# Kernel tuning notes

Measured on AMD Instinct MI355X. Metric: run time of the kernel, lower is better.

Reference implementation:

```python
import jax, jax.numpy as jnp
import numpy as np

B = 8192
T = 100       # repeat_vector
I = 30        # input_size
H = 100       # hidden_size


def setup_inputs() -> dict:
    key = jax.random.key(0)
    ks = jax.random.split(key, 7)
    k = 1.0 / np.sqrt(H)  # torch LSTM/Linear init scale
    u = lambda kk, shape: jax.random.uniform(kk, shape, jnp.float32, -k, k)
    return {
        "x": jax.random.normal(ks[0], (B, I), jnp.float32),
        "W_ih": u(ks[1], (4 * H, I)),   # gate order: i, f, g, o
        "W_hh": u(ks[2], (4 * H, H)),
        "b_ih": u(ks[3], (4 * H,)),
        "b_hh": u(ks[4], (4 * H,)),
        "W_d": u(ks[5], (1, H)),
        "b_d": u(ks[6], (1,)),
    }


def _lstm_dense(x, W_ih, W_hh, b_ih, b_hh, W_d, b_d):
    # Input is the same vector at every timestep (repeat), so project once.
    xp = x @ W_ih.T + b_ih + b_hh  # [B, 4H]
    h0 = jnp.zeros((x.shape[0], H), x.dtype)
    c0 = jnp.zeros((x.shape[0], H), x.dtype)

    def step(carry, _):
        h, c = carry
        gates = xp + h @ W_hh.T                      # [B, 4H]
        i, f, g, o = jnp.split(gates, 4, axis=-1)
        i = jax.nn.sigmoid(i)
        f = jax.nn.sigmoid(f)
        g = jnp.tanh(g)
        o = jax.nn.sigmoid(o)
        c = f * c + i * g
        h = o * jnp.tanh(c)
        return (h, c), h

    _, hs = jax.lax.scan(step, (h0, c0), None, length=T)  # [T, B, H]
    hs = jnp.transpose(hs, (1, 0, 2))                     # [B, T, H]
    return hs @ W_d.T + b_d                               # [B, T, 1]


def reference(x, W_ih, W_hh, b_ih, b_hh, W_d, b_d):
    return _lstm_dense(x, W_ih, W_hh, b_ih, b_hh, W_d, b_d)
```

## Files before the change

kernel.cpp:

```cpp
#include <hip/hip_runtime.h>


#define LOG2E 1.44269504088896340736f

typedef _Float16 f16x8 __attribute__((ext_vector_type(8)));
typedef float    f32x4 __attribute__((ext_vector_type(4)));

__device__ __forceinline__ float rcp_(float x) { return __builtin_amdgcn_rcpf(x); }
__device__ __forceinline__ float exp2_(float x) { return __builtin_amdgcn_exp2f(x); }

__device__ __forceinline__ unsigned pk_f16(float a, float b) {
    return __builtin_bit_cast(unsigned, __builtin_amdgcn_cvt_pkrtz(a, b));
}

#define KS 136

__global__ __launch_bounds__(256, 2) void lstm_kernel(
    const float* __restrict__ x, const float* __restrict__ Wih,
    const float* __restrict__ Whh, const float* __restrict__ bih,
    const float* __restrict__ bhh, const float* __restrict__ Wd,
    const float* __restrict__ bd, float* __restrict__ out)
{
    __shared__ __align__(16) _Float16 Wstg[128 * KS];
    __shared__ __align__(16) _Float16 hlds[2][16 * KS];
    __shared__ float outb[16 * 100];

    const int tid = threadIdx.x;
    const int w   = tid >> 6;
    const int l   = tid & 63;
    const int g   = l >> 4;
    const int c   = l & 15;
    const int b0  = blockIdx.x * 16;
    const bool wpo = (w == 3) && (c == 2);

    for (int i = tid; i < 128 * KS / 2; i += 256) ((unsigned*)Wstg)[i] = 0u;
    for (int i = tid; i < 2 * 16 * KS / 2; i += 256) ((unsigned*)&hlds[0][0])[i] = 0u;
    __syncthreads();

    f16x8 wfrag[2][4][4];
    for (int s = 0; s < 4; ++s) {
        const float sc = (s == 2) ? (-2.0f * LOG2E) : (-LOG2E);
        for (int idx = tid; idx < 10000; idx += 256) {
            int uu = idx / 100, k = idx - uu * 100;
            int col = 32 * (uu >> 5) + 16 * (uu & 1) + ((uu & 31) >> 1);
            Wstg[col * KS + k] = (_Float16)(Whh[(s * 100 + uu) * 100 + k] * sc);
        }
        if (s == 0)
            for (int k = tid; k < 100; k += 256)
                Wstg[98 * KS + k] = (_Float16)Wd[k];
        __syncthreads();
        #pragma unroll
        for (int nt = 0; nt < 2; ++nt)
            #pragma unroll
            for (int ks = 0; ks < 4; ++ks)
                wfrag[nt][s][ks] = *(const f16x8*)
                    &Wstg[(w * 32 + nt * 16 + c) * KS + ks * 32 + g * 8];
        __syncthreads();
    }

    const int row0 = b0 + 4 * g;
    f32x4 xq[2][4];
    float creg[2][4];
    #pragma unroll
    for (int nt = 0; nt < 2; ++nt) {
        #pragma unroll
        for (int s = 0; s < 4; ++s) xq[nt][s] = (f32x4){0.f, 0.f, 0.f, 0.f};
        #pragma unroll
        for (int r = 0; r < 4; ++r) creg[nt][r] = 0.0f;
    }
    for (int k = 0; k < 30; ++k) {
        float xv[4];
        #pragma unroll
        for (int r = 0; r < 4; ++r) xv[r] = x[(row0 + r) * 30 + k];
        #pragma unroll
        for (int nt = 0; nt < 2; ++nt) {
            int u = w * 32 + 2 * c + nt;
            if (u < 100) {
                #pragma unroll
                for (int s = 0; s < 4; ++s) {
                    float wv = Wih[(s * 100 + u) * 30 + k];
                    #pragma unroll
                    for (int r = 0; r < 4; ++r) xq[nt][s][r] += xv[r] * wv;
                }
            }
        }
    }
    #pragma unroll
    for (int nt = 0; nt < 2; ++nt) {
        int u = w * 32 + 2 * c + nt;
        if (u < 100) {
            #pragma unroll
            for (int s = 0; s < 4; ++s) {
                float sc = (s == 2) ? (-2.0f * LOG2E) : (-LOG2E);
                float b  = bih[s * 100 + u] + bhh[s * 100 + u];
                #pragma unroll
                for (int r = 0; r < 4; ++r)
                    xq[nt][s][r] = (xq[nt][s][r] + b) * sc;
            }
        }
    }
    const float bdv = bd[0];
    __syncthreads();

    const int afb = c * KS + g * 8;
    const int hwc = w * 32 + 2 * c;

#define STEP(P, TCUR)                                                          \
    {                                                                          \
        const _Float16* hr = &hlds[(P)][0];                                    \
        _Float16*       hw = &hlds[(P) ^ 1][0];                                \
        f16x8 af[4];                                                           \
        _Pragma("unroll")                                                      \
        for (int ks = 0; ks < 4; ++ks)                                         \
            af[ks] = *(const f16x8*)&hr[afb + ks * 32];                        \
               \
        f32x4 acc[2][4];                                                       \
        _Pragma("unroll")                                                      \
        for (int nt = 0; nt < 2; ++nt)                                         \
            _Pragma("unroll")                                                  \
            for (int s = 0; s < 4; ++s)                                        \
                acc[nt][s] = __builtin_amdgcn_mfma_f32_16x16x32_f16(           \
                        af[0], wfrag[nt][s][0], xq[nt][s], 0, 0, 0);           \
        _Pragma("unroll")                                                      \
        for (int ks = 1; ks < 4; ++ks)                                         \
            _Pragma("unroll")                                                  \
            for (int nt = 0; nt < 2; ++nt)                                     \
                _Pragma("unroll")                                              \
                for (int s = 0; s < 4; ++s)                                    \
                    acc[nt][s] = __builtin_amdgcn_mfma_f32_16x16x32_f16(       \
                            af[ks], wfrag[nt][s][ks], acc[nt][s], 0, 0, 0);    \
              \
        if ((TCUR) > 0 && wpo) {                                               \
            _Pragma("unroll")                                                  \
            for (int r = 0; r < 4; ++r)                                        \
                outb[(4 * g + r) * 100 + (TCUR) - 1] = acc[0][0][r] + bdv;     \
        }                                                                      \
                   \
        _Pragma("unroll")                                                      \
        for (int r = 0; r < 4; ++r) {                                          \
            float hv[2];                                                       \
            _Pragma("unroll")                                                  \
            for (int nt = 0; nt < 2; ++nt) {                                   \
                float A  = exp2_(acc[nt][0][r]);                               \
                float F  = exp2_(acc[nt][1][r]);                               \
                float G  = exp2_(acc[nt][2][r]);                               \
                float O  = exp2_(acc[nt][3][r]);                               \
                float a1 = 1.0f + A, f1 = 1.0f + F;                            \
                float g1 = 1.0f + G, gm = 1.0f - G;                            \
                float ag  = a1 * g1;                                           \
                float num = fmaf(creg[nt][r], ag, gm * f1);                    \
                float cg  = num * rcp_(ag * f1);                               \
                creg[nt][r] = cg;                                              \
                float C2 = exp2_(cg * (-2.0f * LOG2E));                        \
                hv[nt] = (1.0f - C2) * rcp_((1.0f + O) * (1.0f + C2));         \
            }                                                                  \
            *(unsigned*)&hw[(4 * g + r) * KS + hwc] = pk_f16(hv[0], hv[1]);    \
        }                                                                      \
        __syncthreads();                                                       \
    }

    for (int t2 = 0; t2 < 50; ++t2) {
        STEP(0, 2 * t2);
        STEP(1, 2 * t2 + 1);
    }
#undef STEP

    {
        f16x8 af[4];
        #pragma unroll
        for (int ks = 0; ks < 4; ++ks)
            af[ks] = *(const f16x8*)&hlds[0][afb + ks * 32];
        f32x4 a = {0.f, 0.f, 0.f, 0.f};
        #pragma unroll
        for (int ks = 0; ks < 4; ++ks)
            a = __builtin_amdgcn_mfma_f32_16x16x32_f16(
                    af[ks], wfrag[0][0][ks], a, 0, 0, 0);
        if (wpo) {
            #pragma unroll
            for (int r = 0; r < 4; ++r)
                outb[(4 * g + r) * 100 + 99] = a[r] + bdv;
        }
    }
    __syncthreads();
    for (int i = tid; i < 1600; i += 256)
        out[b0 * 100 + i] = outb[i];
}

extern "C" void kernel_launch(void* const* d_in, const int* in_sizes, int n_in,
                              void* d_out, int out_size, void* d_ws, size_t ws_size,
                              hipStream_t stream) {
    (void)in_sizes; (void)n_in; (void)out_size; (void)d_ws; (void)ws_size;
    const float* x   = (const float*)d_in[0];
    const float* Wih = (const float*)d_in[1];
    const float* Whh = (const float*)d_in[2];
    const float* bih = (const float*)d_in[3];
    const float* bhh = (const float*)d_in[4];
    const float* Wd  = (const float*)d_in[5];
    const float* bd  = (const float*)d_in[6];
    lstm_kernel<<<dim3(512), dim3(256), 0, stream>>>(
        x, Wih, Whh, bih, bhh, Wd, bd, (float*)d_out);
}
```

Measured before the change: 172.8 us.

## Process two 16-row batch tiles per block sharing register-resident weight fragments

Each block now handles 32 batch rows as two independent 16-row MFMA tiles that reuse the same W_hh fragments held in registers. The grid is halved to 256 blocks and launch bounds drop to one block per SIMD group. This gives two independent MFMA chains and activation streams per step to hide latency, and halves the number of barriers per row and the per-block weight staging. The cost is higher register pressure and fewer resident waves, and 256 blocks may leave some of the GPU's compute units idle.

```diff
diff --git a/kernel.cpp b/kernel.cpp
--- a/kernel.cpp
+++ b/kernel.cpp
@@ -15,26 +15,26 @@
 
 #define KS 136
 
-__global__ __launch_bounds__(256, 2) void lstm_kernel(
+__global__ __launch_bounds__(256, 1) void lstm_kernel(
     const float* __restrict__ x, const float* __restrict__ Wih,
     const float* __restrict__ Whh, const float* __restrict__ bih,
     const float* __restrict__ bhh, const float* __restrict__ Wd,
     const float* __restrict__ bd, float* __restrict__ out)
 {
     __shared__ __align__(16) _Float16 Wstg[128 * KS];
-    __shared__ __align__(16) _Float16 hlds[2][16 * KS];
-    __shared__ float outb[16 * 100];
+    __shared__ __align__(16) _Float16 hlds[2][32 * KS];
+    __shared__ float outb[32 * 100];
 
     const int tid = threadIdx.x;
     const int w   = tid >> 6;
     const int l   = tid & 63;
     const int g   = l >> 4;
     const int c   = l & 15;
-    const int b0  = blockIdx.x * 16;
+    const int b0  = blockIdx.x * 32;
     const bool wpo = (w == 3) && (c == 2);
 
     for (int i = tid; i < 128 * KS / 2; i += 256) ((unsigned*)Wstg)[i] = 0u;
-    for (int i = tid; i < 2 * 16 * KS / 2; i += 256) ((unsigned*)&hlds[0][0])[i] = 0u;
+    for (int i = tid; i < 2 * 32 * KS / 2; i += 256) ((unsigned*)&hlds[0][0])[i] = 0u;
     __syncthreads();
 
     f16x8 wfrag[2][4][4];
@@ -58,20 +58,25 @@
         __syncthreads();
     }
 
-    const int row0 = b0 + 4 * g;
-    f32x4 xq[2][4];
-    float creg[2][4];
+    f32x4 xqX[2][4], xqY[2][4];
+    float cregX[2][4], cregY[2][4];
     #pragma unroll
     for (int nt = 0; nt < 2; ++nt) {
         #pragma unroll
-        for (int s = 0; s < 4; ++s) xq[nt][s] = (f32x4){0.f, 0.f, 0.f, 0.f};
-        #pragma unroll
-        for (int r = 0; r < 4; ++r) creg[nt][r] = 0.0f;
+        for (int s = 0; s < 4; ++s) {
+            xqX[nt][s] = (f32x4){0.f, 0.f, 0.f, 0.f};
+            xqY[nt][s] = (f32x4){0.f, 0.f, 0.f, 0.f};
+        }
+        #pragma unroll
+        for (int r = 0; r < 4; ++r) { cregX[nt][r] = 0.0f; cregY[nt][r] = 0.0f; }
     }
     for (int k = 0; k < 30; ++k) {
-        float xv[4];
-        #pragma unroll
-        for (int r = 0; r < 4; ++r) xv[r] = x[(row0 + r) * 30 + k];
+        float xvX[4], xvY[4];
+        #pragma unroll
+        for (int r = 0; r < 4; ++r) {
+            xvX[r] = x[(b0 + 4 * g + r) * 30 + k];
+            xvY[r] = x[(b0 + 16 + 4 * g + r) * 30 + k];
+        }
         #pragma unroll
         for (int nt = 0; nt < 2; ++nt) {
             int u = w * 32 + 2 * c + nt;
@@ -80,7 +85,10 @@
                 for (int s = 0; s < 4; ++s) {
                     float wv = Wih[(s * 100 + u) * 30 + k];
                     #pragma unroll
-                    for (int r = 0; r < 4; ++r) xq[nt][s][r] += xv[r] * wv;
+                    for (int r = 0; r < 4; ++r) {
+                        xqX[nt][s][r] += xvX[r] * wv;
+                        xqY[nt][s][r] += xvY[r] * wv;
+                    }
                 }
             }
         }
@@ -94,68 +102,82 @@
                 float sc = (s == 2) ? (-2.0f * LOG2E) : (-LOG2E);
                 float b  = bih[s * 100 + u] + bhh[s * 100 + u];
                 #pragma unroll
-                for (int r = 0; r < 4; ++r)
-                    xq[nt][s][r] = (xq[nt][s][r] + b) * sc;
+                for (int r = 0; r < 4; ++r) {
+                    xqX[nt][s][r] = (xqX[nt][s][r] + b) * sc;
+                    xqY[nt][s][r] = (xqY[nt][s][r] + b) * sc;
+                }
             }
         }
     }
     const float bdv = bd[0];
     __syncthreads();
 
-    const int afb = c * KS + g * 8;
-    const int hwc = w * 32 + 2 * c;
+    const int afbX = c * KS + g * 8;
+    const int afbY = (16 + c) * KS + g * 8;
+    const int hwc  = w * 32 + 2 * c;
+
+#define TILE_ACTS(ACC, CREG, HW, ROWOFF)                                       \
+    _Pragma("unroll")                                                          \
+    for (int r = 0; r < 4; ++r) {                                              \
+        float hv[2];                                                           \
+        _Pragma("unroll")                                                      \
+        for (int nt = 0; nt < 2; ++nt) {                                       \
+            float A  = exp2_(ACC[nt][0][r]);                                   \
+            float F  = exp2_(ACC[nt][1][r]);                                   \
+            float G  = exp2_(ACC[nt][2][r]);                                   \
+            float O  = exp2_(ACC[nt][3][r]);                                   \
+            float a1 = 1.0f + A, f1 = 1.0f + F;                                \
+            float g1 = 1.0f + G, gm = 1.0f - G;                                \
+            float ag  = a1 * g1;                                               \
+            float num = fmaf(CREG[nt][r], ag, gm * f1);                        \
+            float cg  = num * rcp_(ag * f1);                                   \
+            CREG[nt][r] = cg;                                                  \
+            float C2 = exp2_(cg * (-2.0f * LOG2E));                            \
+            hv[nt] = (1.0f - C2) * rcp_((1.0f + O) * (1.0f + C2));             \
+        }                                                                      \
+        *(unsigned*)&HW[((ROWOFF) + 4 * g + r) * KS + hwc] = pk_f16(hv[0], hv[1]); \
+    }
 
 #define STEP(P, TCUR)                                                          \
     {                                                                          \
         const _Float16* hr = &hlds[(P)][0];                                    \
         _Float16*       hw = &hlds[(P) ^ 1][0];                                \
-        f16x8 af[4];                                                           \
-        _Pragma("unroll")                                                      \
-        for (int ks = 0; ks < 4; ++ks)                                         \
-            af[ks] = *(const f16x8*)&hr[afb + ks * 32];                        \
-               \
-        f32x4 acc[2][4];                                                       \
+        f16x8 afX[4], afY[4];                                                  \
+        _Pragma("unroll")                                                      \
+        for (int ks = 0; ks < 4; ++ks) {                                       \
+            afX[ks] = *(const f16x8*)&hr[afbX + ks * 32];                      \
+            afY[ks] = *(const f16x8*)&hr[afbY + ks * 32];                      \
+        }                                                                      \
+        f32x4 accX[2][4], accY[2][4];                                          \
         _Pragma("unroll")                                                      \
         for (int nt = 0; nt < 2; ++nt)                                         \
             _Pragma("unroll")                                                  \
-            for (int s = 0; s < 4; ++s)                                        \
-                acc[nt][s] = __builtin_amdgcn_mfma_f32_16x16x32_f16(           \
-                        af[0], wfrag[nt][s][0], xq[nt][s], 0, 0, 0);           \
+            for (int s = 0; s < 4; ++s) {                                      \
+                accX[nt][s] = __builtin_amdgcn_mfma_f32_16x16x32_f16(          \
+                        afX[0], wfrag[nt][s][0], xqX[nt][s], 0, 0, 0);         \
+                accY[nt][s] = __builtin_amdgcn_mfma_f32_16x16x32_f16(          \
+                        afY[0], wfrag[nt][s][0], xqY[nt][s], 0, 0, 0);         \
+            }                                                                  \
         _Pragma("unroll")                                                      \
         for (int ks = 1; ks < 4; ++ks)                                         \
             _Pragma("unroll")                                                  \
             for (int nt = 0; nt < 2; ++nt)                                     \
                 _Pragma("unroll")                                              \
-                for (int s = 0; s < 4; ++s)                                    \
-                    acc[nt][s] = __builtin_amdgcn_mfma_f32_16x16x32_f16(       \
-                            af[ks], wfrag[nt][s][ks], acc[nt][s], 0, 0, 0);    \
-              \
+                for (int s = 0; s < 4; ++s) {                                  \
+                    accX[nt][s] = __builtin_amdgcn_mfma_f32_16x16x32_f16(      \
+                            afX[ks], wfrag[nt][s][ks], accX[nt][s], 0, 0, 0);  \
+                    accY[nt][s] = __builtin_amdgcn_mfma_f32_16x16x32_f16(      \
+                            afY[ks], wfrag[nt][s][ks], accY[nt][s], 0, 0, 0);  \
+                }                                                              \
         if ((TCUR) > 0 && wpo) {                                               \
             _Pragma("unroll")                                                  \
-            for (int r = 0; r < 4; ++r)                                        \
-                outb[(4 * g + r) * 100 + (TCUR) - 1] = acc[0][0][r] + bdv;     \
+            for (int r = 0; r < 4; ++r) {                                      \
+                outb[(4 * g + r) * 100 + (TCUR) - 1] = accX[0][0][r] + bdv;    \
+                outb[(16 + 4 * g + r) * 100 + (TCUR) - 1] = accY[0][0][r] + bdv; \
+            }                                                                  \
         }                                                                      \
-                   \
-        _Pragma("unroll")                                                      \
-        for (int r = 0; r < 4; ++r) {                                          \
-            float hv[2];                                                       \
-            _Pragma("unroll")                                                  \
-            for (int nt = 0; nt < 2; ++nt) {                                   \
-                float A  = exp2_(acc[nt][0][r]);                               \
-                float F  = exp2_(acc[nt][1][r]);                               \
-                float G  = exp2_(acc[nt][2][r]);                               \
-                float O  = exp2_(acc[nt][3][r]);                               \
-                float a1 = 1.0f + A, f1 = 1.0f + F;                            \
-                float g1 = 1.0f + G, gm = 1.0f - G;                            \
-                float ag  = a1 * g1;                                           \
-                float num = fmaf(creg[nt][r], ag, gm * f1);                    \
-                float cg  = num * rcp_(ag * f1);                               \
-                creg[nt][r] = cg;                                              \
-                float C2 = exp2_(cg * (-2.0f * LOG2E));                        \
-                hv[nt] = (1.0f - C2) * rcp_((1.0f + O) * (1.0f + C2));         \
-            }                                                                  \
-            *(unsigned*)&hw[(4 * g + r) * KS + hwc] = pk_f16(hv[0], hv[1]);    \
-        }                                                                      \
+        TILE_ACTS(accX, cregX, hw, 0)                                          \
+        TILE_ACTS(accY, cregY, hw, 16)                                         \
         __syncthreads();                                                       \
     }
 
@@ -164,25 +186,31 @@
         STEP(1, 2 * t2 + 1);
     }
 #undef STEP
+#undef TILE_ACTS
 
     {
-        f16x8 af[4];
-        #pragma unroll
-        for (int ks = 0; ks < 4; ++ks)
-            af[ks] = *(const f16x8*)&hlds[0][afb + ks * 32];
-        f32x4 a = {0.f, 0.f, 0.f, 0.f};
-        #pragma unroll
-        for (int ks = 0; ks < 4; ++ks)
-            a = __builtin_amdgcn_mfma_f32_16x16x32_f16(
-                    af[ks], wfrag[0][0][ks], a, 0, 0, 0);
+        f16x8 afX[4], afY[4];
+        #pragma unroll
+        for (int ks = 0; ks < 4; ++ks) {
+            afX[ks] = *(const f16x8*)&hlds[0][afbX + ks * 32];
+            afY[ks] = *(const f16x8*)&hlds[0][afbY + ks * 32];
+        }
+        f32x4 aX = {0.f, 0.f, 0.f, 0.f}, aY = {0.f, 0.f, 0.f, 0.f};
+        #pragma unroll
+        for (int ks = 0; ks < 4; ++ks) {
+            aX = __builtin_amdgcn_mfma_f32_16x16x32_f16(afX[ks], wfrag[0][0][ks], aX, 0, 0, 0);
+            aY = __builtin_amdgcn_mfma_f32_16x16x32_f16(afY[ks], wfrag[0][0][ks], aY, 0, 0, 0);
+        }
         if (wpo) {
             #pragma unroll
-            for (int r = 0; r < 4; ++r)
-                outb[(4 * g + r) * 100 + 99] = a[r] + bdv;
+            for (int r = 0; r < 4; ++r) {
+                outb[(4 * g + r) * 100 + 99] = aX[r] + bdv;
+                outb[(16 + 4 * g + r) * 100 + 99] = aY[r] + bdv;
+            }
         }
     }
     __syncthreads();
-    for (int i = tid; i < 1600; i += 256)
+    for (int i = tid; i < 3200; i += 256)
         out[b0 * 100 + i] = outb[i];
 }
 
@@ -197,6 +225,6 @@
     const float* bhh = (const float*)d_in[4];
     const float* Wd  = (const float*)d_in[5];
     const float* bd  = (const float*)d_in[6];
-    lstm_kernel<<<dim3(512), dim3(256), 0, stream>>>(
+    lstm_kernel<<<dim3(256), dim3(256), 0, stream>>>(
         x, Wih, Whh, bih, bhh, Wd, bd, (float*)d_out);
 }
```

Result: slower. 187.2 us (+8.4%).
